# Kernel optimization log

Hardware: AMD Instinct MI355X
Metric: run time of the kernel (lower is better)

Reference implementation:

```python
import jax, jax.numpy as jnp
import numpy as np
import math

NUM_HEADS = 8
NUM_CHANNELS = 512
B, C, H, W = 8, 512, 32, 32
LN_EPS = 1e-6


def setup_inputs() -> dict:
    key = jax.random.key(0)
    ks = jax.random.split(key, 7)
    s = 1.0 / math.sqrt(NUM_CHANNELS)
    return {
        "key": jax.random.normal(ks[0], (B, C, H, W), jnp.float32),
        "value": jax.random.normal(ks[1], (B, C, H, W), jnp.float32),
        "query": jax.random.normal(ks[2], (B, C, H, W), jnp.float32),
        "Wq": jax.random.normal(ks[3], (C, C), jnp.float32) * s,
        "Wk": jax.random.normal(ks[4], (C, C), jnp.float32) * s,
        "Wv": jax.random.normal(ks[5], (C, C), jnp.float32) * s,
        "Wo": jax.random.normal(ks[6], (C, C), jnp.float32) * s,
        "ln_gamma": jnp.ones((C,), jnp.float32),
        "ln_beta": jnp.zeros((C,), jnp.float32),
    }


def _to_tokens(x):
    # b c h w -> b (h w) c
    b, c, h, w = x.shape
    return x.transpose(0, 2, 3, 1).reshape(b, h * w, c)


def _split_heads(x, m):
    # (B, HW, C) -> (B, m, HW, d); matches reshape (B,HW,m,d) then 'b hw m d -> (b m) hw d'
    b, hw, c = x.shape
    d = c // m
    return x.reshape(b, hw, m, d).transpose(0, 2, 1, 3)


def _merge_heads_cm(x):
    # (B, m, HW, d) -> (B, HW, d*m) with channel index = c*m + head  ('(b m) hw c -> b hw (c m)')
    b, m, hw, d = x.shape
    return x.transpose(0, 2, 3, 1).reshape(b, hw, d * m)


def reference(key, value, query, Wq, Wk, Wv, Wo, ln_gamma, ln_beta):
    m = NUM_HEADS
    b, c, h, w = query.shape
    d = c // m

    q = _to_tokens(query) @ Wq.T  # (B, HW, C)
    k = _to_tokens(key) @ Wk.T
    v = _to_tokens(value) @ Wv.T

    qh = _split_heads(q, m)  # (B, m, HW, d)
    kh = _split_heads(k, m)
    vh = _split_heads(v, m)

    scores = jnp.einsum('bmqd,bmkd->bmqk', qh, kh) / math.sqrt(d)
    p_attn = jax.nn.softmax(scores, axis=-1)
    out = jnp.einsum('bmqk,bmkd->bmqd', p_attn, vh)  # (B, m, HW, d)

    out = _merge_heads_cm(out)        # (B, HW, C) interleaved as (c m)
    residual = _merge_heads_cm(qh)    # same interleaving of projected query

    x = out + residual
    mu = jnp.mean(x, axis=-1, keepdims=True)
    var = jnp.mean(jnp.square(x - mu), axis=-1, keepdims=True)
    x = (x - mu) / jnp.sqrt(var + LN_EPS) * ln_gamma + ln_beta

    x = x @ Wo.T  # (B, HW, C)
    return x.reshape(b, h, w, c).transpose(0, 3, 1, 2)  # b (h w) c -> b c h w
```

## Files before the change

kernel.cpp:

```cpp
#include <hip/hip_runtime.h>
#include <stdint.h>

typedef __bf16 bf16x8 __attribute__((ext_vector_type(8)));
typedef float f32x4 __attribute__((ext_vector_type(4)));
typedef unsigned short u16x4 __attribute__((ext_vector_type(4)));
typedef unsigned short u16x8 __attribute__((ext_vector_type(8)));

#define MFMA16(a, b, c) __builtin_amdgcn_mfma_f32_16x16x32_bf16(a, b, c, 0, 0, 0)

__device__ __forceinline__ unsigned short f2bf(float f) {
  union { float f; unsigned u; } v; v.f = f;
  unsigned r = v.u + 0x7fffu + ((v.u >> 16) & 1u);
  return (unsigned short)(r >> 16);
}
__device__ __forceinline__ float bf2f(unsigned short h) {
  union { unsigned u; float f; } v; v.u = ((unsigned)h) << 16; return v.f;
}
__device__ __forceinline__ unsigned pk2(float a, float b) {
  union { float f; unsigned u; } x, y; x.f = a; y.f = b;
  unsigned ra = x.u + 0x7fffu + ((x.u >> 16) & 1u);
  unsigned rb = y.u + 0x7fffu + ((y.u >> 16) & 1u);
  return (ra >> 16) | (rb & 0xffff0000u);
}
__device__ __forceinline__ void gload16(const void* g, void* l) {
  __builtin_amdgcn_global_load_lds(
      (const __attribute__((address_space(1))) void*)g,
      (__attribute__((address_space(3))) void*)l, 16, 0, 0);
}
__device__ __forceinline__ float fexp2(float x) {
#if __has_builtin(__builtin_amdgcn_exp2f)
  return __builtin_amdgcn_exp2f(x);
#else
  return exp2f(x);
#endif
}

__global__ __launch_bounds__(256) void wconv_kernel(
    const float* __restrict__ w0, const float* __restrict__ w1,
    const float* __restrict__ w2, const float* __restrict__ w3,
    unsigned short* __restrict__ o0, unsigned short* __restrict__ o1,
    unsigned short* __restrict__ o2, unsigned short* __restrict__ o3) {
  int z = blockIdx.y;
  const float* s = z == 0 ? w0 : z == 1 ? w1 : z == 2 ? w2 : w3;
  unsigned short* d = z == 0 ? o0 : z == 1 ? o1 : z == 2 ? o2 : o3;
  int t = blockIdx.x * 256 + threadIdx.x;
  const f32x4* sp = (const f32x4*)(s + (size_t)t * 8);
  f32x4 a = sp[0], b = sp[1];
  u16x8 r;
  r[0] = f2bf(a[0]); r[1] = f2bf(a[1]); r[2] = f2bf(a[2]); r[3] = f2bf(a[3]);
  r[4] = f2bf(b[0]); r[5] = f2bf(b[1]); r[6] = f2bf(b[2]); r[7] = f2bf(b[3]);
  *(u16x8*)(d + (size_t)t * 8) = r;
}

__global__ __launch_bounds__(256, 3) void gemm_qkv(
    const float* __restrict__ X0, const float* __restrict__ X1,
    const float* __restrict__ X2,
    const unsigned short* __restrict__ B0, const unsigned short* __restrict__ B1,
    const unsigned short* __restrict__ B2,
    unsigned short* __restrict__ O0, unsigned short* __restrict__ O1,
    unsigned short* __restrict__ O2) {
  __shared__ float aTf[2][4096];
  __shared__ unsigned short bT[2][4096];
  int z = blockIdx.y;
  const float* X = z == 0 ? X0 : z == 1 ? X1 : X2;
  const unsigned short* BT = z == 0 ? B0 : z == 1 ? B1 : B2;
  int j = blockIdx.x;
  int bm = (j & 7) * 8 + (j >> 5);
  int bn = (j >> 3) & 3;
  int tid = threadIdx.x, lane = tid & 63, w = tid >> 6;
  int wr = w >> 1, wc = w & 1, l15 = lane & 15, lhi = lane >> 4;
  const int m0 = bm * 128, n0 = bn * 128;
  const int b512 = (m0 >> 10) * 512;
  const int hw0 = m0 & 1023;

  const float* asf[4];
  int adoff[4];
#pragma unroll
  for (int i = 0; i < 4; ++i) {
    int u = i * 256 + tid;
    int ch = u >> 5, pc = u & 31;
    int lc = pc ^ ((ch >> 3) & 3);
    asf[i] = X + (size_t)(b512 + ch) * 1024 + hw0 + lc * 4;
    adoff[i] = u * 4;
  }
  int u0 = tid, u1 = 256 + tid;
  int br0 = u0 >> 2, bc0 = (u0 & 3) ^ (br0 & 3);
  int br1 = u1 >> 2, bc1 = (u1 & 3) ^ (br1 & 3);
  const unsigned short* bsrc0 = BT + (size_t)(n0 + br0) * 512 + bc0 * 8;
  const unsigned short* bsrc1 = BT + (size_t)(n0 + br1) * 512 + bc1 * 8;

#define QSTAGE(bufi, it)                                            \
  do {                                                              \
    gload16(asf[0] + (it) * 32768, &aTf[bufi][adoff[0]]);           \
    gload16(asf[1] + (it) * 32768, &aTf[bufi][adoff[1]]);           \
    gload16(asf[2] + (it) * 32768, &aTf[bufi][adoff[2]]);           \
    gload16(asf[3] + (it) * 32768, &aTf[bufi][adoff[3]]);           \
    gload16(bsrc0 + (it) * 32, &bT[bufi][u0 * 8]);                  \
    gload16(bsrc1 + (it) * 32, &bT[bufi][u1 * 8]);                  \
  } while (0)

  int aoffA[4];
#pragma unroll
  for (int mi = 0; mi < 4; ++mi) {
    int tok = wr * 64 + mi * 16 + l15;
    int atok = ((((tok >> 2) ^ lhi) << 2) | (tok & 3));
    aoffA[mi] = lhi * 1024 + atok;
  }
  int boff[4];
#pragma unroll
  for (int i = 0; i < 4; ++i) {
    int brow = wc * 64 + i * 16 + l15;
    boff[i] = brow * 32 + ((lhi ^ (brow & 3)) * 8);
  }

  f32x4 acc[4][4] = {};

#define QTILE(BUF, IT)                                                        \
  do {                                                                       \
    if ((IT) + 1 < 16) QSTAGE((BUF) ^ 1, (IT) + 1);                           \
    bf16x8 af[4], bfr[4];                                                    \
    _Pragma("unroll") for (int mi = 0; mi < 4; ++mi) {                        \
      union { unsigned u[4]; bf16x8 v; } ap;                                  \
      float a0 = aTf[BUF][aoffA[mi] + 0 * 128];                               \
      float a1 = aTf[BUF][aoffA[mi] + 1 * 128];                               \
      float a2 = aTf[BUF][aoffA[mi] + 2 * 128];                               \
      float a3 = aTf[BUF][aoffA[mi] + 3 * 128];                               \
      float a4 = aTf[BUF][aoffA[mi] + 4 * 128];                               \
      float a5 = aTf[BUF][aoffA[mi] + 5 * 128];                               \
      float a6 = aTf[BUF][aoffA[mi] + 6 * 128];                               \
      float a7 = aTf[BUF][aoffA[mi] + 7 * 128];                               \
      ap.u[0] = pk2(a0, a1); ap.u[1] = pk2(a2, a3);                           \
      ap.u[2] = pk2(a4, a5); ap.u[3] = pk2(a6, a7);                           \
      af[mi] = ap.v;                                                          \
    }                                                                         \
    _Pragma("unroll") for (int ni = 0; ni < 4; ++ni)                          \
        bfr[ni] = *(const bf16x8*)&bT[BUF][boff[ni]];                         \
    __builtin_amdgcn_s_setprio(1);                                           \
    _Pragma("unroll") for (int mi = 0; mi < 4; ++mi)                          \
        _Pragma("unroll") for (int ni = 0; ni < 4; ++ni)                      \
            acc[mi][ni] = MFMA16(af[mi], bfr[ni], acc[mi][ni]);               \
    __builtin_amdgcn_s_setprio(0);                                           \
    __syncthreads();                                                         \
  } while (0)

  QSTAGE(0, 0);
  __syncthreads();
  for (int it2 = 0; it2 < 16; it2 += 2) {
    QTILE(0, it2);
    QTILE(1, it2 + 1);
  }
#undef QTILE
#undef QSTAGE

  float sc = (z == 1) ? (0.125f * 1.44269504f) : 1.0f;
#pragma unroll
  for (int mi = 0; mi < 4; ++mi) {
#pragma unroll
    for (int ni = 0; ni < 4; ++ni) {
      int row = m0 + wr * 64 + mi * 16 + lhi * 4;
      int col = n0 + wc * 64 + ni * 16 + l15;
      if (z < 2) {
        unsigned short* C = z == 0 ? O0 : O1;
#pragma unroll
        for (int j2 = 0; j2 < 4; ++j2)
          C[(size_t)(row + j2) * 512 + col] = f2bf(acc[mi][ni][j2] * sc);
      } else {
        int bb = row >> 10, hw = row & 1023;
        u16x4 p;
        p[0] = f2bf(acc[mi][ni][0]); p[1] = f2bf(acc[mi][ni][1]);
        p[2] = f2bf(acc[mi][ni][2]); p[3] = f2bf(acc[mi][ni][3]);
        *(u16x4*)&O2[(size_t)bb * 524288 + (size_t)col * 1024 + hw] = p;
      }
    }
  }
}

__global__ __launch_bounds__(256, 4) void gemm_out(const unsigned short* __restrict__ A,
                                                   const unsigned short* __restrict__ BT,
                                                   float* __restrict__ C) {
  __shared__ unsigned short aT[2][128 * 32];
  __shared__ unsigned short bT[2][64 * 32];
  int j = blockIdx.x;
  int bm = (j & 7) * 8 + (j >> 6);
  int bn = (j >> 3) & 7;
  int tid = threadIdx.x, lane = tid & 63, w = tid >> 6;
  int l15 = lane & 15, lhi = lane >> 4;
  const int m0 = bm * 128, n0 = bn * 64;

  int u0 = tid, u1 = 256 + tid;
  int ar0 = u0 >> 2, ac0 = (u0 & 3) ^ (ar0 & 3);
  int ar1 = u1 >> 2, ac1 = (u1 & 3) ^ (ar1 & 3);
  const unsigned short* asrc0 = A + (size_t)(m0 + ar0) * 512 + ac0 * 8;
  const unsigned short* asrc1 = A + (size_t)(m0 + ar1) * 512 + ac1 * 8;
  const unsigned short* bsrc0 = BT + (size_t)(n0 + ar0) * 512 + ac0 * 8;

#define OSTAGE(bufi, it)                                     \
  do {                                                       \
    gload16(asrc0 + (it) * 32, &aT[bufi][u0 * 8]);           \
    gload16(asrc1 + (it) * 32, &aT[bufi][u1 * 8]);           \
    gload16(bsrc0 + (it) * 32, &bT[bufi][u0 * 8]);           \
  } while (0)

  int aoff[2], boff[4];
#pragma unroll
  for (int i = 0; i < 2; ++i) {
    int arow = w * 32 + i * 16 + l15;
    aoff[i] = arow * 32 + ((lhi ^ (arow & 3)) * 8);
  }
#pragma unroll
  for (int i = 0; i < 4; ++i) {
    int brow = i * 16 + l15;
    boff[i] = brow * 32 + ((lhi ^ (brow & 3)) * 8);
  }

  f32x4 acc[2][4] = {};

#define OTILE(BUF, IT)                                                        \
  do {                                                                       \
    if ((IT) + 1 < 16) OSTAGE((BUF) ^ 1, (IT) + 1);                           \
    bf16x8 af[2], bfr[4];                                                    \
    _Pragma("unroll") for (int mi = 0; mi < 2; ++mi)                          \
        af[mi] = *(const bf16x8*)&aT[BUF][aoff[mi]];                          \
    _Pragma("unroll") for (int ni = 0; ni < 4; ++ni)                          \
        bfr[ni] = *(const bf16x8*)&bT[BUF][boff[ni]];                         \
    __builtin_amdgcn_s_setprio(1);                                           \
    _Pragma("unroll") for (int mi = 0; mi < 2; ++mi)                          \
        _Pragma("unroll") for (int ni = 0; ni < 4; ++ni)                      \
            acc[mi][ni] = MFMA16(af[mi], bfr[ni], acc[mi][ni]);               \
    __builtin_amdgcn_s_setprio(0);                                           \
    __syncthreads();                                                         \
  } while (0)

  OSTAGE(0, 0);
  __syncthreads();
  for (int it2 = 0; it2 < 16; it2 += 2) {
    OTILE(0, it2);
    OTILE(1, it2 + 1);
  }
#undef OTILE
#undef OSTAGE

#pragma unroll
  for (int mi = 0; mi < 2; ++mi) {
#pragma unroll
    for (int ni = 0; ni < 4; ++ni) {
      int row = m0 + w * 32 + mi * 16 + lhi * 4;
      int col = n0 + ni * 16 + l15;
      int bb = row >> 10, hw = row & 1023;
      *(f32x4*)&C[(size_t)bb * 524288 + (size_t)col * 1024 + hw] = acc[mi][ni];
    }
  }
}

__global__ __launch_bounds__(256, 2) void attn_kernel(
    const unsigned short* __restrict__ q_tok, const unsigned short* __restrict__ k_tok,
    const unsigned short* __restrict__ v_cm, unsigned short* __restrict__ y_hm) {
  __shared__ unsigned short k_lds[2][64 * 64];
  __shared__ unsigned short v_lds[2][64 * 64];
  __shared__ unsigned short p_lds[4][2][16 * 64];

  int bid = blockIdx.x;
  int slot = bid >> 3;
  int bh = (bid & 7) * 8 + (slot >> 3);
  int qb = slot & 7;
  int h = bh & 7, b = bh >> 3;
  int tid = threadIdx.x;
  int lane = tid & 63, w = tid >> 6;
  int l15 = lane & 15, lhi = lane >> 4;

  const unsigned short* kbase = k_tok + (size_t)b * 524288 + h * 64;
  const unsigned short* vbase = v_cm + (size_t)b * 524288 + (size_t)h * 65536;

  int qglob0 = b * 1024 + qb * 128 + w * 32;
  bf16x8 qf[2][2];
#pragma unroll
  for (int sub = 0; sub < 2; ++sub) {
    const unsigned short* qp =
        q_tok + (size_t)(qglob0 + sub * 16 + l15) * 512 + h * 64 + lhi * 8;
    qf[sub][0] = *(const bf16x8*)qp;
    qf[sub][1] = *(const bf16x8*)(qp + 32);
  }

  bf16x8 ones;
#pragma unroll
  for (int i = 0; i < 8; ++i) ones[i] = (__bf16)1.0f;

  int u0 = tid, u1 = 256 + tid;
  int r0 = u0 >> 3, c0 = (u0 & 7) ^ (r0 & 7);
  int r1 = u1 >> 3, c1 = (u1 & 7) ^ (r1 & 7);
  const unsigned short* ksrc0 = kbase + (size_t)r0 * 512 + c0 * 8;
  const unsigned short* ksrc1 = kbase + (size_t)r1 * 512 + c1 * 8;
  const unsigned short* vsrc0 = vbase + (size_t)r0 * 1024 + c0 * 8;
  const unsigned short* vsrc1 = vbase + (size_t)r1 * 1024 + c1 * 8;

#define STAGE(bufi, kti)                                                    \
  do {                                                                      \
    gload16(ksrc0 + (size_t)(kti) * 32768, &k_lds[bufi][u0 * 8]);           \
    gload16(ksrc1 + (size_t)(kti) * 32768, &k_lds[bufi][u1 * 8]);           \
    gload16(vsrc0 + (kti) * 64, &v_lds[bufi][u0 * 8]);                      \
    gload16(vsrc1 + (kti) * 64, &v_lds[bufi][u1 * 8]);                      \
  } while (0)

  int kvoff[4][2];
#pragma unroll
  for (int nt = 0; nt < 4; ++nt) {
    int brow = nt * 16 + l15, sw = brow & 7;
    kvoff[nt][0] = brow * 64 + ((lhi ^ sw) * 8);
    kvoff[nt][1] = brow * 64 + (((4 + lhi) ^ sw) * 8);
  }

  char* pb = (char*)&p_lds[w][0][0];
  int p2 = (l15 & 7) << 1;
  char* pwr[2][4];
  const char* prd[2][2];
#pragma unroll
  for (int sub = 0; sub < 2; ++sub) {
#pragma unroll
    for (int nt = 0; nt < 4; ++nt)
      pwr[sub][nt] = pb + sub * 2048 + l15 * 128 + ((((nt << 2) | lhi) ^ p2) << 3);
#pragma unroll
    for (int kc = 0; kc < 2; ++kc)
      prd[sub][kc] = pb + sub * 2048 + l15 * 128 + ((((kc << 3) | (lhi << 1)) ^ p2) << 3);
  }

  f32x4 ls[2] = {{0.f, 0.f, 0.f, 0.f}, {0.f, 0.f, 0.f, 0.f}};
  f32x4 o[2][4] = {};

#define TILE(BUF, KT)                                                        \
  do {                                                                       \
    if ((KT) + 1 < 16) STAGE((BUF) ^ 1, (KT) + 1);                           \
    const unsigned short* kl = k_lds[BUF];                                   \
    const unsigned short* vl = v_lds[BUF];                                   \
    f32x4 st[2][4];                                                          \
    __builtin_amdgcn_s_setprio(1);                                           \
    _Pragma("unroll") for (int nt = 0; nt < 4; ++nt) {                       \
      bf16x8 kf0 = *(const bf16x8*)&kl[kvoff[nt][0]];                        \
      bf16x8 kf1 = *(const bf16x8*)&kl[kvoff[nt][1]];                        \
      _Pragma("unroll") for (int sub = 0; sub < 2; ++sub) {                  \
        f32x4 a = {0.f, 0.f, 0.f, 0.f};                                      \
        a = MFMA16(kf0, qf[sub][0], a);                                      \
        a = MFMA16(kf1, qf[sub][1], a);                                      \
        st[sub][nt] = a;                                                     \
      }                                                                      \
    }                                                                        \
    __builtin_amdgcn_s_setprio(0);                                           \
    bf16x8 vf[4][2];                                                         \
    _Pragma("unroll") for (int dt = 0; dt < 4; ++dt) {                       \
      vf[dt][0] = *(const bf16x8*)&vl[kvoff[dt][0]];                         \
      vf[dt][1] = *(const bf16x8*)&vl[kvoff[dt][1]];                         \
    }                                                                        \
    _Pragma("unroll") for (int sub = 0; sub < 2; ++sub) {                    \
      _Pragma("unroll") for (int nt = 0; nt < 4; ++nt) {                     \
        float e0 = fexp2(st[sub][nt][0]);                                    \
        float e1 = fexp2(st[sub][nt][1]);                                    \
        float e2 = fexp2(st[sub][nt][2]);                                    \
        float e3 = fexp2(st[sub][nt][3]);                                    \
        uint2 pk;                                                            \
        pk.x = pk2(e0, e1);                                                  \
        pk.y = pk2(e2, e3);                                                  \
        *(uint2*)pwr[sub][nt] = pk;                                          \
      }                                                                      \
    }                                                                        \
    asm volatile("" ::: "memory");                                          \
    bf16x8 pf[2][2];                                                         \
    _Pragma("unroll") for (int sub = 0; sub < 2; ++sub) {                    \
      pf[sub][0] = *(const bf16x8*)prd[sub][0];                              \
      pf[sub][1] = *(const bf16x8*)prd[sub][1];                              \
    }                                                                        \
    __builtin_amdgcn_s_setprio(1);                                           \
    _Pragma("unroll") for (int dt = 0; dt < 4; ++dt) {                       \
      _Pragma("unroll") for (int sub = 0; sub < 2; ++sub) {                  \
        o[sub][dt] = MFMA16(pf[sub][0], vf[dt][0], o[sub][dt]);              \
        o[sub][dt] = MFMA16(pf[sub][1], vf[dt][1], o[sub][dt]);              \
      }                                                                      \
    }                                                                        \
    _Pragma("unroll") for (int sub = 0; sub < 2; ++sub) {                    \
      ls[sub] = MFMA16(pf[sub][0], ones, ls[sub]);                           \
      ls[sub] = MFMA16(pf[sub][1], ones, ls[sub]);                           \
    }                                                                        \
    __builtin_amdgcn_s_setprio(0);                                           \
    __syncthreads();                                                         \
  } while (0)

  STAGE(0, 0);
  __syncthreads();
  for (int kt2 = 0; kt2 < 16; kt2 += 2) {
    TILE(0, kt2);
    TILE(1, kt2 + 1);
  }
#undef TILE
#undef STAGE

#pragma unroll
  for (int sub = 0; sub < 2; ++sub) {
    float inv[4];
#pragma unroll
    for (int r = 0; r < 4; ++r) inv[r] = 1.0f / ls[sub][r];
#pragma unroll
    for (int dt = 0; dt < 4; ++dt) {
#pragma unroll
      for (int r = 0; r < 4; ++r) {
        int q = qglob0 + sub * 16 + lhi * 4 + r;
        size_t idx = (size_t)q * 512 + h * 64 + dt * 16 + l15;
        float res = bf2f(q_tok[idx]);
        y_hm[idx] = f2bf(o[sub][dt][r] * inv[r] + res);
      }
    }
  }
}

__global__ __launch_bounds__(256) void ln_kernel(
    const unsigned short* __restrict__ y_hm,
    const float* __restrict__ gamma, const float* __restrict__ beta,
    unsigned short* __restrict__ xln) {
  __shared__ float y_s[512];
  __shared__ float red[8];
  int row = blockIdx.x;
  int t = threadIdx.x;
  float y0 = bf2f(y_hm[(size_t)row * 512 + t]);
  float y1 = bf2f(y_hm[(size_t)row * 512 + 256 + t]);
  y_s[t] = y0;
  y_s[t + 256] = y1;
  float s = y0 + y1, ss = y0 * y0 + y1 * y1;
#pragma unroll
  for (int msk = 1; msk < 64; msk <<= 1) {
    s += __shfl_xor(s, msk);
    ss += __shfl_xor(ss, msk);
  }
  int w = t >> 6, lane = t & 63;
  if (lane == 0) { red[w] = s; red[4 + w] = ss; }
  __syncthreads();
  s = (red[0] + red[1]) + (red[2] + red[3]);
  ss = (red[4] + red[5]) + (red[6] + red[7]);
  float mean = s * (1.0f / 512.0f);
  float var = ss * (1.0f / 512.0f) - mean * mean;
  float rstd = rsqrtf(var + 1e-6f);
  int c0 = t, c1 = t + 256;
  int p0 = ((c0 & 7) << 6) | (c0 >> 3);
  int p1 = ((c1 & 7) << 6) | (c1 >> 3);
  xln[(size_t)row * 512 + c0] = f2bf((y_s[p0] - mean) * rstd * gamma[c0] + beta[c0]);
  xln[(size_t)row * 512 + c1] = f2bf((y_s[p1] - mean) * rstd * gamma[c1] + beta[c1]);
}

extern "C" void kernel_launch(void* const* d_in, const int* in_sizes, int n_in,
                              void* d_out, int out_size, void* d_ws, size_t ws_size,
                              hipStream_t stream) {
  const float* key   = (const float*)d_in[0];
  const float* value = (const float*)d_in[1];
  const float* query = (const float*)d_in[2];
  const float* Wq = (const float*)d_in[3];
  const float* Wk = (const float*)d_in[4];
  const float* Wv = (const float*)d_in[5];
  const float* Wo = (const float*)d_in[6];
  const float* gamma = (const float*)d_in[7];
  const float* beta  = (const float*)d_in[8];

  char* ws = (char*)d_ws;
  unsigned short* Wq_b = (unsigned short*)(ws);
  unsigned short* Wk_b = Wq_b + 262144;
  unsigned short* Wv_b = Wk_b + 262144;
  unsigned short* Wo_b = Wv_b + 262144;
  unsigned short* q_tok = (unsigned short*)(ws + (size_t)(26u) * 1048576);
  unsigned short* k_tok = (unsigned short*)(ws + (size_t)(34u) * 1048576);
  unsigned short* v_cm  = (unsigned short*)(ws + (size_t)(42u) * 1048576);
  unsigned short* xln   = (unsigned short*)(ws + (size_t)(2u) * 1048576);
  unsigned short* y_hm  = (unsigned short*)d_out;

  wconv_kernel<<<dim3(128, 4), 256, 0, stream>>>(Wq, Wk, Wv, Wo, Wq_b, Wk_b, Wv_b, Wo_b);
  gemm_qkv<<<dim3(256, 3), 256, 0, stream>>>(query, key, value, Wq_b, Wk_b, Wv_b,
                                             q_tok, k_tok, v_cm);
  attn_kernel<<<512, 256, 0, stream>>>(q_tok, k_tok, v_cm, y_hm);
  ln_kernel<<<8192, 256, 0, stream>>>(y_hm, gamma, beta, xln);
  gemm_out<<<512, 256, 0, stream>>>(xln, Wo_b, (float*)d_out);
}
```

Measured before the change: 87.15 us.

## Convert QKV GEMM A-tile to bf16 via registers before LDS staging

```diff
diff --git a/kernel.cpp b/kernel.cpp
--- a/kernel.cpp
+++ b/kernel.cpp
@@ -21,6 +21,12 @@
   unsigned ra = x.u + 0x7fffu + ((x.u >> 16) & 1u);
   unsigned rb = y.u + 0x7fffu + ((y.u >> 16) & 1u);
   return (ra >> 16) | (rb & 0xffff0000u);
+}
+__device__ __forceinline__ unsigned pk2c(float a, float b) {
+  union { unsigned u; __bf16 h[2]; } v;
+  v.h[0] = (__bf16)a;
+  v.h[1] = (__bf16)b;
+  return v.u;
 }
 __device__ __forceinline__ void gload16(const void* g, void* l) {
   __builtin_amdgcn_global_load_lds(
@@ -59,8 +65,8 @@
     const unsigned short* __restrict__ B2,
     unsigned short* __restrict__ O0, unsigned short* __restrict__ O1,
     unsigned short* __restrict__ O2) {
-  __shared__ float aTf[2][4096];
-  __shared__ unsigned short bT[2][4096];
+  __shared__ unsigned short aB[2][128 * 40];
+  __shared__ unsigned short bT[2][128 * 32];
   int z = blockIdx.y;
   const float* X = z == 0 ? X0 : z == 1 ? X1 : X2;
   const unsigned short* BT = z == 0 ? B0 : z == 1 ? B1 : B2;
@@ -73,38 +79,24 @@
   const int b512 = (m0 >> 10) * 512;
   const int hw0 = m0 & 1023;
 
-  const float* asf[4];
-  int adoff[4];
-#pragma unroll
-  for (int i = 0; i < 4; ++i) {
-    int u = i * 256 + tid;
-    int ch = u >> 5, pc = u & 31;
-    int lc = pc ^ ((ch >> 3) & 3);
-    asf[i] = X + (size_t)(b512 + ch) * 1024 + hw0 + lc * 4;
-    adoff[i] = u * 4;
-  }
+  int tok0 = (tid & 31) * 4;
+  int ch0 = (tid >> 5) * 4;
+  const float* xbase = X + (size_t)(b512 + ch0) * 1024 + hw0 + tok0;
+  int Kw = ((tid & 31) >> 2) & 6;
+  int aw0 = tok0 * 40 + (((ch0 >> 2) ^ Kw) << 2);
+
   int u0 = tid, u1 = 256 + tid;
   int br0 = u0 >> 2, bc0 = (u0 & 3) ^ (br0 & 3);
   int br1 = u1 >> 2, bc1 = (u1 & 3) ^ (br1 & 3);
   const unsigned short* bsrc0 = BT + (size_t)(n0 + br0) * 512 + bc0 * 8;
   const unsigned short* bsrc1 = BT + (size_t)(n0 + br1) * 512 + bc1 * 8;
 
-#define QSTAGE(bufi, it)                                            \
-  do {                                                              \
-    gload16(asf[0] + (it) * 32768, &aTf[bufi][adoff[0]]);           \
-    gload16(asf[1] + (it) * 32768, &aTf[bufi][adoff[1]]);           \
-    gload16(asf[2] + (it) * 32768, &aTf[bufi][adoff[2]]);           \
-    gload16(asf[3] + (it) * 32768, &aTf[bufi][adoff[3]]);           \
-    gload16(bsrc0 + (it) * 32, &bT[bufi][u0 * 8]);                  \
-    gload16(bsrc1 + (it) * 32, &bT[bufi][u1 * 8]);                  \
-  } while (0)
-
-  int aoffA[4];
+  int aoff[4];
 #pragma unroll
   for (int mi = 0; mi < 4; ++mi) {
-    int tok = wr * 64 + mi * 16 + l15;
-    int atok = ((((tok >> 2) ^ lhi) << 2) | (tok & 3));
-    aoffA[mi] = lhi * 1024 + atok;
+    int T0 = wr * 64 + mi * 16;
+    int kap = ((wr * 4 + mi) >> 1) & 3;
+    aoff[mi] = (T0 + l15) * 40 + ((lhi ^ kap) << 3);
   }
   int boff[4];
 #pragma unroll
@@ -113,26 +105,43 @@
     boff[i] = brow * 32 + ((lhi ^ (brow & 3)) * 8);
   }
 
+  f32x4 xr0, xr1, xr2, xr3;
+
+#define ALOAD(it)                                                      \
+  do {                                                                 \
+    xr0 = *(const f32x4*)(xbase + ((it) * 32 + 0) * 1024);             \
+    xr1 = *(const f32x4*)(xbase + ((it) * 32 + 1) * 1024);             \
+    xr2 = *(const f32x4*)(xbase + ((it) * 32 + 2) * 1024);             \
+    xr3 = *(const f32x4*)(xbase + ((it) * 32 + 3) * 1024);             \
+  } while (0)
+
+#define AWRITE(bufi)                                                   \
+  do {                                                                 \
+    _Pragma("unroll") for (int i = 0; i < 4; ++i) {                    \
+      uint2 pv;                                                        \
+      pv.x = pk2c(xr0[i], xr1[i]);                                     \
+      pv.y = pk2c(xr2[i], xr3[i]);                                     \
+      *(uint2*)&aB[bufi][aw0 + i * 40] = pv;                           \
+    }                                                                  \
+  } while (0)
+
+#define BSTAGE(bufi, it)                                               \
+  do {                                                                 \
+    gload16(bsrc0 + (it) * 32, &bT[bufi][u0 * 8]);                     \
+    gload16(bsrc1 + (it) * 32, &bT[bufi][u1 * 8]);                     \
+  } while (0)
+
   f32x4 acc[4][4] = {};
 
 #define QTILE(BUF, IT)                                                        \
   do {                                                                       \
-    if ((IT) + 1 < 16) QSTAGE((BUF) ^ 1, (IT) + 1);                           \
+    if ((IT) + 1 < 16) {                                                     \
+      ALOAD((IT) + 1);                                                       \
+      BSTAGE((BUF) ^ 1, (IT) + 1);                                           \
+    }                                                                        \
     bf16x8 af[4], bfr[4];                                                    \
-    _Pragma("unroll") for (int mi = 0; mi < 4; ++mi) {                        \
-      union { unsigned u[4]; bf16x8 v; } ap;                                  \
-      float a0 = aTf[BUF][aoffA[mi] + 0 * 128];                               \
-      float a1 = aTf[BUF][aoffA[mi] + 1 * 128];                               \
-      float a2 = aTf[BUF][aoffA[mi] + 2 * 128];                               \
-      float a3 = aTf[BUF][aoffA[mi] + 3 * 128];                               \
-      float a4 = aTf[BUF][aoffA[mi] + 4 * 128];                               \
-      float a5 = aTf[BUF][aoffA[mi] + 5 * 128];                               \
-      float a6 = aTf[BUF][aoffA[mi] + 6 * 128];                               \
-      float a7 = aTf[BUF][aoffA[mi] + 7 * 128];                               \
-      ap.u[0] = pk2(a0, a1); ap.u[1] = pk2(a2, a3);                           \
-      ap.u[2] = pk2(a4, a5); ap.u[3] = pk2(a6, a7);                           \
-      af[mi] = ap.v;                                                          \
-    }                                                                         \
+    _Pragma("unroll") for (int mi = 0; mi < 4; ++mi)                          \
+        af[mi] = *(const bf16x8*)&aB[BUF][aoff[mi]];                          \
     _Pragma("unroll") for (int ni = 0; ni < 4; ++ni)                          \
         bfr[ni] = *(const bf16x8*)&bT[BUF][boff[ni]];                         \
     __builtin_amdgcn_s_setprio(1);                                           \
@@ -140,17 +149,22 @@
         _Pragma("unroll") for (int ni = 0; ni < 4; ++ni)                      \
             acc[mi][ni] = MFMA16(af[mi], bfr[ni], acc[mi][ni]);               \
     __builtin_amdgcn_s_setprio(0);                                           \
+    if ((IT) + 1 < 16) AWRITE((BUF) ^ 1);    \
     __syncthreads();                                                         \
   } while (0)
 
-  QSTAGE(0, 0);
+  ALOAD(0);
+  BSTAGE(0, 0);
+  AWRITE(0);
   __syncthreads();
   for (int it2 = 0; it2 < 16; it2 += 2) {
     QTILE(0, it2);
     QTILE(1, it2 + 1);
   }
 #undef QTILE
-#undef QSTAGE
+#undef ALOAD
+#undef AWRITE
+#undef BSTAGE
 
   float sc = (z == 1) ? (0.125f * 1.44269504f) : 1.0f;
 #pragma unroll
```

Result: faster. 83.48 us, median of 5 (-4.2%).
